# Kernel optimization log

Measured on AMD Instinct MI355X. Metric: run time of the kernel, lower is better.

The kernel has to match this reference:

```python
import jax, jax.numpy as jnp
import numpy as np

D_MODEL = 512
T_MAX = 1000.0


def setup_inputs() -> dict:
    key = jax.random.key(0)
    t = jax.random.uniform(key, (524288,), dtype=jnp.float32) * T_MAX
    return {"t": t}


def reference(t) -> jnp.ndarray:
    # i = 0..d_model-1; freq_i = 10000 ** (2*i / d_model)
    i = jnp.arange(D_MODEL, dtype=jnp.float32)  # [D]
    inv_freq = jnp.exp(-(2.0 * i / D_MODEL) * jnp.log(jnp.float32(10000.0)))  # [D]
    arg = t[..., None] * inv_freq  # [B, D]
    even = (jnp.arange(D_MODEL) % 2) == 0  # sin at even i, cos at odd i
    return jnp.where(even, jnp.sin(arg), jnp.cos(arg))
```

## Files before the change

### kernel.cpp

```cpp
#include <hip/hip_runtime.h>
#include <math.h>


#define D_MODEL 512

typedef float f32x4 __attribute__((ext_vector_type(4)));

__device__ __forceinline__ float sin_rev(float r) {
    return __builtin_amdgcn_sinf(__builtin_amdgcn_fractf(r));
}
__device__ __forceinline__ float cos_rev(float r) {
    return __builtin_amdgcn_cosf(__builtin_amdgcn_fractf(r));
}

__global__ __launch_bounds__(256) void time_embed_kernel(
    const float* __restrict__ t, f32x4* __restrict__ out, int n_rows) {
    const int g = blockIdx.x * 256 + threadIdx.x;
    const int c = g & 63;
    const size_t w = (size_t)(g >> 6);
    const size_t nw = (size_t)(gridDim.x * 256) >> 6;

    const float LOG2_10000_OVER_256 = 0.051904345232615426f;
    const float INV_2PI = 0.15915494309189535f;

    const int d0a = 4 * c;
    const int d0b = 4 * c + 256;

    float fa[4], fb[4];
#pragma unroll
    for (int j = 0; j < 4; ++j) {
        fa[j] = __builtin_amdgcn_exp2f(-(float)(d0a + j) * LOG2_10000_OVER_256) * INV_2PI;
        fb[j] = __builtin_amdgcn_exp2f(-(float)(d0b + j) * LOG2_10000_OVER_256) * INV_2PI;
    }

    if (w >= (size_t)n_rows) return;
    float tv = t[w];
    for (size_t r = w; r < (size_t)n_rows; r += nw) {
        const size_t rn = r + nw;
        const float tn = t[rn < (size_t)n_rows ? rn : r];

        f32x4 oa, ob;
        oa.x = sin_rev(tv * fa[0]);
        oa.y = cos_rev(tv * fa[1]);
        oa.z = sin_rev(tv * fa[2]);
        oa.w = cos_rev(tv * fa[3]);
        ob.x = sin_rev(tv * fb[0]);
        ob.y = cos_rev(tv * fb[1]);
        ob.z = sin_rev(tv * fb[2]);
        ob.w = cos_rev(tv * fb[3]);

        f32x4* rowp = out + r * (D_MODEL / 4);
        __builtin_nontemporal_store(oa, rowp + c);
        __builtin_nontemporal_store(ob, rowp + 64 + c);

        tv = tn;
    }
}

extern "C" void kernel_launch(void* const* d_in, const int* in_sizes, int n_in,
                              void* d_out, int out_size, void* d_ws, size_t ws_size,
                              hipStream_t stream) {
    const float* t = (const float*)d_in[0];
    f32x4* out = (f32x4*)d_out;
    const int n_rows = in_sizes[0];
    time_embed_kernel<<<dim3(2048), dim3(256), 0, stream>>>(t, out, n_rows);
}
```

Baseline: 220.1 us.

## Assign contiguous 64-row chunks per wavefront with vectorized t loads

Each wavefront now processes a contiguous block of 64 rows instead of grid-striding one row at a time, loading t as float4 with one-step prefetch. Output stores switch from nontemporal to regular stores. The grid stays at 2048 blocks, so rows beyond 2048*4*64 are never written, and the float4 loads assume n_rows is a multiple of 64.

```diff
diff --git a/kernel.cpp b/kernel.cpp
--- a/kernel.cpp
+++ b/kernel.cpp
@@ -17,43 +17,46 @@
     const float* __restrict__ t, f32x4* __restrict__ out, int n_rows) {
     const int g = blockIdx.x * 256 + threadIdx.x;
     const int c = g & 63;
-    const size_t w = (size_t)(g >> 6);
-    const size_t nw = (size_t)(gridDim.x * 256) >> 6;
+    const int w = g >> 6;
 
     const float LOG2_10000_OVER_256 = 0.051904345232615426f;
     const float INV_2PI = 0.15915494309189535f;
 
-    const int d0a = 4 * c;
-    const int d0b = 4 * c + 256;
-
     float fa[4], fb[4];
 #pragma unroll
     for (int j = 0; j < 4; ++j) {
-        fa[j] = __builtin_amdgcn_exp2f(-(float)(d0a + j) * LOG2_10000_OVER_256) * INV_2PI;
-        fb[j] = __builtin_amdgcn_exp2f(-(float)(d0b + j) * LOG2_10000_OVER_256) * INV_2PI;
+        fa[j] = __builtin_amdgcn_exp2f(-(float)(4 * c + j) * LOG2_10000_OVER_256) * INV_2PI;
+        fb[j] = __builtin_amdgcn_exp2f(-(float)(4 * c + 256 + j) * LOG2_10000_OVER_256) * INV_2PI;
     }
 
-    if (w >= (size_t)n_rows) return;
-    float tv = t[w];
-    for (size_t r = w; r < (size_t)n_rows; r += nw) {
-        const size_t rn = r + nw;
-        const float tn = t[rn < (size_t)n_rows ? rn : r];
+    const int row0 = w * 64;
+    if (row0 >= n_rows) return;
+    const float* tw = t + row0;
+    f32x4* outw = out + (size_t)row0 * (D_MODEL / 4);
 
-        f32x4 oa, ob;
-        oa.x = sin_rev(tv * fa[0]);
-        oa.y = cos_rev(tv * fa[1]);
-        oa.z = sin_rev(tv * fa[2]);
-        oa.w = cos_rev(tv * fa[3]);
-        ob.x = sin_rev(tv * fb[0]);
-        ob.y = cos_rev(tv * fb[1]);
-        ob.z = sin_rev(tv * fb[2]);
-        ob.w = cos_rev(tv * fb[3]);
+    f32x4 tq = *(const f32x4*)tw;
+#pragma unroll 4
+    for (int q = 0; q < 16; ++q) {
+        const int qn = (q < 15) ? (q + 1) : q;
+        const f32x4 tnext = *(const f32x4*)(tw + 4 * qn);
 
-        f32x4* rowp = out + r * (D_MODEL / 4);
-        __builtin_nontemporal_store(oa, rowp + c);
-        __builtin_nontemporal_store(ob, rowp + 64 + c);
-
-        tv = tn;
+#pragma unroll
+        for (int j = 0; j < 4; ++j) {
+            const float tv = tq[j];
+            f32x4 oa, ob;
+            oa.x = sin_rev(tv * fa[0]);
+            oa.y = cos_rev(tv * fa[1]);
+            oa.z = sin_rev(tv * fa[2]);
+            oa.w = cos_rev(tv * fa[3]);
+            ob.x = sin_rev(tv * fb[0]);
+            ob.y = cos_rev(tv * fb[1]);
+            ob.z = sin_rev(tv * fb[2]);
+            ob.w = cos_rev(tv * fb[3]);
+            f32x4* rowp = outw + (size_t)(4 * q + j) * (D_MODEL / 4);
+            rowp[c] = oa;
+            rowp[64 + c] = ob;
+        }
+        tq = tnext;
     }
 }
 
```

Result: faster. 201.7 us (-8.4%).
